# Optimization experiments

Measured on AMD Instinct MI355X. Metric: run time of the kernel, lower is better.

The kernel has to match this reference:

```python
import jax, jax.numpy as jnp
import numpy as np

THR = 1.0     # snntorch Leaky default threshold
BETA = 0.9    # args.beta
ALPHA = 2.0   # surrogate.atan default alpha

@jax.custom_vjp
def atan_spike(x):
    # Heaviside forward, arctan surrogate gradient (snntorch surrogate.atan)
    return (x > 0).astype(x.dtype)

def _aspk_fwd(x):
    return atan_spike(x), x

def _aspk_bwd(x, g):
    return (g * (ALPHA / 2.0) / (1.0 + (jnp.pi / 2.0 * ALPHA * x) ** 2),)

atan_spike.defvjp(_aspk_fwd, _aspk_bwd)

def setup_inputs() -> dict:
    key = jax.random.key(0)
    k = jax.random.split(key, 5)
    B, D, H, C = 32768, 187, 50, 5
    return {
        "x": jax.random.normal(k[0], (B, D), dtype=jnp.float32),
        "W1": jax.random.normal(k[1], (H, D), dtype=jnp.float32) * (1.0 / np.sqrt(D)),
        "b1": jax.random.normal(k[2], (H,), dtype=jnp.float32) * 0.01,
        "W2": jax.random.normal(k[3], (C, H), dtype=jnp.float32) * (1.0 / np.sqrt(H)),
        "b2": jax.random.normal(k[4], (C,), dtype=jnp.float32) * 0.01,
        "num_steps": 100,
    }

def reference(x, W1, b1, W2, b2, num_steps):
    B = x.shape[0]
    dt = x.dtype
    # fc1(x) is identical every timestep (x is static), compute once
    cur1 = x @ W1.T + b1  # [B, 50]

    def step(carry, _):
        mem1, mem2 = carry
        # Leaky: reset computed from PREVIOUS mem (detached), subtract mechanism
        reset1 = jax.lax.stop_gradient((mem1 > THR).astype(dt))
        mem1 = BETA * mem1 + cur1 - reset1 * THR
        spk1 = atan_spike(mem1 - THR)
        cur2 = spk1 @ W2.T + b2  # [B, num_classes]
        reset2 = jax.lax.stop_gradient((mem2 > THR).astype(dt))
        mem2 = BETA * mem2 + cur2 - reset2 * THR
        spk2 = atan_spike(mem2 - THR)
        return (mem1, mem2), (spk2, mem2)

    init = (jnp.zeros((B, W1.shape[0]), dt), jnp.zeros((B, W2.shape[0]), dt))
    _, (spk_rec, mem_rec) = jax.lax.scan(step, init, None, length=num_steps)
    return spk_rec, mem_rec  # each [num_steps, B, num_classes]
```

## Files before the change

### kernel.cpp

```cpp
#include <hip/hip_runtime.h>

typedef float v2f __attribute__((ext_vector_type(2)));

#define DD   187
#define HH   50
#define PH   56
#define HPJ  28
#define NP   14
#define NC   5
#define RPB  128
#define BLK  256
#define DCH  64
#define NCHUNK 3
#define BETA 0.9f

__device__ __forceinline__ float dpp_xor1(float v) {
    return __builtin_bit_cast(float,
        __builtin_amdgcn_mov_dpp(__builtin_bit_cast(int, v), 0xB1, 0xF, 0xF, true));
}

__device__ __forceinline__ v2f spike2(v2f m) {
    const v2f BIG2  = { 0x1.0p60f,  0x1.0p60f};
    const v2f NBIG2 = {-0x1.0p60f, -0x1.0p60f};
    const v2f ONE2  = {1.f, 1.f};
    const v2f ZERO2 = {0.f, 0.f};
    v2f t = __builtin_elementwise_fma(m, BIG2, NBIG2);
    return __builtin_elementwise_min(__builtin_elementwise_max(t, ZERO2), ONE2);
}

__global__ __launch_bounds__(BLK, 1)
void snn_kernel(const float* __restrict__ x,
                const float* __restrict__ W1,
                const float* __restrict__ b1,
                const float* __restrict__ W2,
                const float* __restrict__ b2,
                const int*   __restrict__ nsp,
                float* __restrict__ out, int Brows)
{
    __shared__ float xs[RPB * 65];
    __shared__ float w1t[DCH * PH];

    const int tid = threadIdx.x;
    const int p   = tid >> 1;
    const int j   = tid & 1;
    const int row = blockIdx.x * RPB + p;
    const int NS  = nsp[0];

    v2f acc[NP];
#pragma unroll
    for (int i = 0; i < NP; ++i) acc[i] = (v2f){0.f, 0.f};

    for (int ch = 0; ch < NCHUNK; ++ch) {
        const int d0 = ch * DCH;
        for (int i = tid; i < RPB * DCH; i += BLK) {
            int r = i >> 6, dd = i & 63;
            int d = d0 + dd;
            xs[r * 65 + dd] = (d < DD) ? x[(size_t)(blockIdx.x * RPB + r) * DD + d] : 0.f;
        }
        for (int i = tid; i < DCH * PH; i += BLK) {
            int h = i >> 6, dd = i & 63;
            int d = d0 + dd;
            w1t[dd * PH + h] = (h < HH && d < DD) ? W1[h * DD + d] : 0.f;
        }
        __syncthreads();

        const float* xr = xs + p * 65;
#pragma unroll 4
        for (int d = 0; d < DCH; ++d) {
            float xv = xr[d];
            const v2f* wr = (const v2f*)(w1t + d * PH + j * HPJ);
            v2f xvv = {xv, xv};
#pragma unroll
            for (int i = 0; i < NP; ++i)
                acc[i] = __builtin_elementwise_fma(xvv, wr[i], acc[i]);
        }
        __syncthreads();
    }

    v2f c1[NP];
#pragma unroll
    for (int i = 0; i < NP; ++i) {
        int h0 = j * HPJ + 2 * i;
        v2f bb = { (h0     < HH) ? b1[h0]     : 0.f,
                   (h0 + 1 < HH) ? b1[h0 + 1] : 0.f };
        c1[i] = acc[i] + bb;
    }

    v2f w2r[NC][NP];
#pragma unroll
    for (int c = 0; c < NC; ++c)
#pragma unroll
        for (int i = 0; i < NP; ++i) {
            int h0 = j * HPJ + 2 * i;
            w2r[c][i] = { (h0     < HH) ? W2[c * HH + h0]     : 0.f,
                          (h0 + 1 < HH) ? W2[c * HH + h0 + 1] : 0.f };
        }
    float b2r[NC];
#pragma unroll
    for (int c = 0; c < NC; ++c) b2r[c] = b2[c];

    v2f m1[NP], s1[NP];
#pragma unroll
    for (int i = 0; i < NP; ++i) { m1[i] = (v2f){0.f, 0.f}; s1[i] = (v2f){0.f, 0.f}; }
    float m2[NC];
#pragma unroll
    for (int c = 0; c < NC; ++c) m2[c] = 0.f;

    const size_t stepStride = (size_t)Brows * NC;
    float* optr = out + (size_t)row * NC + (j ? (size_t)NS * stepStride : 0);
    const v2f BETA2 = {BETA, BETA};

    for (int t = 0; t < NS; ++t) {
        v2f cp0 = {0.f,0.f}, cp1 = {0.f,0.f}, cp2 = {0.f,0.f}, cp3 = {0.f,0.f}, cp4 = {0.f,0.f};
#pragma unroll
        for (int i = 0; i < NP; ++i) {
            v2f m = __builtin_elementwise_fma(BETA2, m1[i], c1[i]) - s1[i];
            m1[i] = m;
            v2f s = spike2(m);
            s1[i] = s;
            cp0 = __builtin_elementwise_fma(s, w2r[0][i], cp0);
            cp1 = __builtin_elementwise_fma(s, w2r[1][i], cp1);
            cp2 = __builtin_elementwise_fma(s, w2r[2][i], cp2);
            cp3 = __builtin_elementwise_fma(s, w2r[3][i], cp3);
            cp4 = __builtin_elementwise_fma(s, w2r[4][i], cp4);
        }
        float cur2[NC];
        cur2[0] = cp0.x + cp0.y; cur2[1] = cp1.x + cp1.y; cur2[2] = cp2.x + cp2.y;
        cur2[3] = cp3.x + cp3.y; cur2[4] = cp4.x + cp4.y;
#pragma unroll
        for (int c = 0; c < NC; ++c) {
            float v = cur2[c];
            v += dpp_xor1(v);
            cur2[c] = v + b2r[c];
        }
#pragma unroll
        for (int c = 0; c < NC; ++c) {
            float mv = m2[c];
            float rp = (mv > 1.f) ? 1.f : 0.f;
            mv = fmaf(BETA, mv, cur2[c]) - rp;
            m2[c] = mv;
            float s2 = (mv > 1.f) ? 1.f : 0.f;
            optr[c] = j ? mv : s2;
        }
        optr += stepStride;
    }
}

extern "C" void kernel_launch(void* const* d_in, const int* in_sizes, int n_in,
                              void* d_out, int out_size, void* d_ws, size_t ws_size,
                              hipStream_t stream) {
    const float* x  = (const float*)d_in[0];
    const float* W1 = (const float*)d_in[1];
    const float* b1 = (const float*)d_in[2];
    const float* W2 = (const float*)d_in[3];
    const float* b2 = (const float*)d_in[4];
    const int*   ns = (const int*)d_in[5];
    int B = in_sizes[0] / DD;
    int nblocks = B / RPB;
    snn_kernel<<<nblocks, BLK, 0, stream>>>(x, W1, b1, W2, b2, ns, (float*)d_out, B);
}
```

Baseline: 218.6 us.

## Split each row across four lanes and distribute output stores per lane

Each batch row is now handled by four threads instead of two. Every lane owns 14 hidden units (7 packed pairs), and the partial sums are reduced with two DPP steps. Rows per block are halved and launch bounds now allow two blocks per CU, which cuts per-thread registers and should raise occupancy. The output layer is split so each lane updates and stores one class, with lane 0 also handling class 4, instead of one lane writing all spikes and the other all membranes. The cost is more redundant layer-1 membrane work per row, an extra shuffle, and less even per-lane store work.

```diff
diff --git a/kernel.cpp b/kernel.cpp
--- a/kernel.cpp
+++ b/kernel.cpp
@@ -5,10 +5,10 @@
 #define DD   187
 #define HH   50
 #define PH   56
-#define HPJ  28
-#define NP   14
+#define HPJ  14
+#define NP   7
 #define NC   5
-#define RPB  128
+#define RPB  64
 #define BLK  256
 #define DCH  64
 #define NCHUNK 3
@@ -18,7 +18,15 @@
     return __builtin_bit_cast(float,
         __builtin_amdgcn_mov_dpp(__builtin_bit_cast(int, v), 0xB1, 0xF, 0xF, true));
 }
+__device__ __forceinline__ float dpp_xor2(float v) {
+    return __builtin_bit_cast(float,
+        __builtin_amdgcn_mov_dpp(__builtin_bit_cast(int, v), 0x4E, 0xF, 0xF, true));
+}
 
+__device__ __forceinline__ float spike1(float m) {
+    float t = fmaf(m, 0x1.0p60f, -0x1.0p60f);
+    return fminf(fmaxf(t, 0.f), 1.f);
+}
 __device__ __forceinline__ v2f spike2(v2f m) {
     const v2f BIG2  = { 0x1.0p60f,  0x1.0p60f};
     const v2f NBIG2 = {-0x1.0p60f, -0x1.0p60f};
@@ -28,7 +36,7 @@
     return __builtin_elementwise_min(__builtin_elementwise_max(t, ZERO2), ONE2);
 }
 
-__global__ __launch_bounds__(BLK, 1)
+__global__ __launch_bounds__(BLK, 2)
 void snn_kernel(const float* __restrict__ x,
                 const float* __restrict__ W1,
                 const float* __restrict__ b1,
@@ -41,8 +49,8 @@
     __shared__ float w1t[DCH * PH];
 
     const int tid = threadIdx.x;
-    const int p   = tid >> 1;
-    const int j   = tid & 1;
+    const int p   = tid >> 2;
+    const int k   = tid & 3;
     const int row = blockIdx.x * RPB + p;
     const int NS  = nsp[0];
 
@@ -68,7 +76,7 @@
 #pragma unroll 4
         for (int d = 0; d < DCH; ++d) {
             float xv = xr[d];
-            const v2f* wr = (const v2f*)(w1t + d * PH + j * HPJ);
+            const v2f* wr = (const v2f*)(w1t + d * PH + k * HPJ);
             v2f xvv = {xv, xv};
 #pragma unroll
             for (int i = 0; i < NP; ++i)
@@ -80,7 +88,7 @@
     v2f c1[NP];
 #pragma unroll
     for (int i = 0; i < NP; ++i) {
-        int h0 = j * HPJ + 2 * i;
+        int h0 = k * HPJ + 2 * i;
         v2f bb = { (h0     < HH) ? b1[h0]     : 0.f,
                    (h0 + 1 < HH) ? b1[h0 + 1] : 0.f };
         c1[i] = acc[i] + bb;
@@ -91,58 +99,61 @@
     for (int c = 0; c < NC; ++c)
 #pragma unroll
         for (int i = 0; i < NP; ++i) {
-            int h0 = j * HPJ + 2 * i;
+            int h0 = k * HPJ + 2 * i;
             w2r[c][i] = { (h0     < HH) ? W2[c * HH + h0]     : 0.f,
                           (h0 + 1 < HH) ? W2[c * HH + h0 + 1] : 0.f };
         }
-    float b2r[NC];
-#pragma unroll
-    for (int c = 0; c < NC; ++c) b2r[c] = b2[c];
+    const float b2A = b2[k];
+    const float b2B = b2[4];
 
     v2f m1[NP], s1[NP];
 #pragma unroll
     for (int i = 0; i < NP; ++i) { m1[i] = (v2f){0.f, 0.f}; s1[i] = (v2f){0.f, 0.f}; }
-    float m2[NC];
-#pragma unroll
-    for (int c = 0; c < NC; ++c) m2[c] = 0.f;
+    float mA = 0.f, sA = 0.f, mB = 0.f, sB = 0.f;
 
-    const size_t stepStride = (size_t)Brows * NC;
-    float* optr = out + (size_t)row * NC + (j ? (size_t)NS * stepStride : 0);
+    const size_t stride = (size_t)Brows * NC;
+    float* spkBase = out;
+    float* memBase = out + (size_t)NS * stride;
+    const int offA = row * NC + k;
+    const int offB = row * NC + 4;
     const v2f BETA2 = {BETA, BETA};
 
     for (int t = 0; t < NS; ++t) {
-        v2f cp0 = {0.f,0.f}, cp1 = {0.f,0.f}, cp2 = {0.f,0.f}, cp3 = {0.f,0.f}, cp4 = {0.f,0.f};
+        v2f cp[NC];
+#pragma unroll
+        for (int c = 0; c < NC; ++c) cp[c] = (v2f){0.f, 0.f};
 #pragma unroll
         for (int i = 0; i < NP; ++i) {
             v2f m = __builtin_elementwise_fma(BETA2, m1[i], c1[i]) - s1[i];
             m1[i] = m;
             v2f s = spike2(m);
             s1[i] = s;
-            cp0 = __builtin_elementwise_fma(s, w2r[0][i], cp0);
-            cp1 = __builtin_elementwise_fma(s, w2r[1][i], cp1);
-            cp2 = __builtin_elementwise_fma(s, w2r[2][i], cp2);
-            cp3 = __builtin_elementwise_fma(s, w2r[3][i], cp3);
-            cp4 = __builtin_elementwise_fma(s, w2r[4][i], cp4);
+#pragma unroll
+            for (int c = 0; c < NC; ++c)
+                cp[c] = __builtin_elementwise_fma(s, w2r[c][i], cp[c]);
         }
         float cur2[NC];
-        cur2[0] = cp0.x + cp0.y; cur2[1] = cp1.x + cp1.y; cur2[2] = cp2.x + cp2.y;
-        cur2[3] = cp3.x + cp3.y; cur2[4] = cp4.x + cp4.y;
 #pragma unroll
         for (int c = 0; c < NC; ++c) {
-            float v = cur2[c];
-            v += dpp_xor1(v);
-            cur2[c] = v + b2r[c];
+            float r = cp[c].x + cp[c].y;
+            r += dpp_xor1(r);
+            r += dpp_xor2(r);
+            cur2[c] = r;
         }
-#pragma unroll
-        for (int c = 0; c < NC; ++c) {
-            float mv = m2[c];
-            float rp = (mv > 1.f) ? 1.f : 0.f;
-            mv = fmaf(BETA, mv, cur2[c]) - rp;
-            m2[c] = mv;
-            float s2 = (mv > 1.f) ? 1.f : 0.f;
-            optr[c] = j ? mv : s2;
-        }
-        optr += stepStride;
+        float cA = (k == 0) ? cur2[0] : (k == 1) ? cur2[1] : (k == 2) ? cur2[2] : cur2[3];
+        float cB = cur2[4];
+
+        mA = fmaf(BETA, mA, cA + b2A) - sA;
+        sA = spike1(mA);
+        mB = fmaf(BETA, mB, cB + b2B) - sB;
+        sB = spike1(mB);
+
+        spkBase[offA] = sA;
+        memBase[offA] = mA;
+        if (k == 0) { spkBase[offB] = sB; memBase[offB] = mB; }
+
+        spkBase += stride;
+        memBase += stride;
     }
 }
 
```

Result: no change. 215.9 us (-1.2%).
